# Performance work log

Hardware: AMD Instinct MI355X
Metric: run time of the kernel (lower is better)

The kernel has to match this reference:

```python
import jax, jax.numpy as jnp
import numpy as np

BN_EPS = 1e-5

def setup_inputs() -> dict:
    key = jax.random.key(0)
    B, C, T, N = 64, 1, 1024, 512
    weighted_fmri = jax.random.normal(key, (B, C, T, N), dtype=jnp.float32)
    bn_weight = jnp.ones((1,), dtype=jnp.float32)   # BatchNorm2d(1) affine weight
    bn_bias = jnp.zeros((1,), dtype=jnp.float32)    # BatchNorm2d(1) affine bias
    return {"weighted_fmri": weighted_fmri, "bn_weight": bn_weight, "bn_bias": bn_bias}


def reference(weighted_fmri, bn_weight, bn_bias):
    # weighted_fmri: [B, 1, T, N]. Original applies BatchNorm2d(1) per-sample
    # (batch of size 1 in training mode => normalize each sample by its own
    # mean/biased-var over (T, N)), then corrcoef over ROIs (columns).
    x = weighted_fmri
    mean = jnp.mean(x, axis=(1, 2, 3), keepdims=True)           # [B,1,1,1]
    var = jnp.mean((x - mean) ** 2, axis=(1, 2, 3), keepdims=True)  # biased var
    w = bn_weight.reshape(1, -1, 1, 1)
    b = bn_bias.reshape(1, -1, 1, 1)
    y = (x - mean) * jax.lax.rsqrt(var + BN_EPS) * w + b        # [B,1,T,N]

    X = y[:, 0]                                                 # [B,T,N]
    T = X.shape[1]
    # corrcoef(X.T): variables = N ROIs, observations = T timepoints
    Xc = X - jnp.mean(X, axis=1, keepdims=True)                 # center over time
    cov = jnp.einsum("btn,btm->bnm", Xc, Xc) / (T - 1)          # [B,N,N]
    d = jnp.sqrt(jnp.diagonal(cov, axis1=1, axis2=2))           # [B,N]
    corr = cov / (d[:, :, None] * d[:, None, :])
    return jnp.clip(corr, -1.0, 1.0)                            # [B,N,N]
```

## Files before the change

kernel.cpp:

```cpp
#include <hip/hip_runtime.h>
#include <hip/hip_bf16.h>

typedef __attribute__((ext_vector_type(8))) short bf16x8;
typedef __attribute__((ext_vector_type(4))) short s16x4;
typedef __attribute__((ext_vector_type(4))) float f32x4;

#define B_ 64
#define T_ 1024
#define N_ 512

#define FENCE() asm volatile("" ::: "memory")
#define VMWAIT(N) asm volatile("s_waitcnt vmcnt(" #N ")" ::: "memory")
#define BAR() __builtin_amdgcn_s_barrier()

__device__ __forceinline__ void async16(const void* g, void* l) {
  __builtin_amdgcn_global_load_lds(
      (const __attribute__((address_space(1))) unsigned int*)g,
      (__attribute__((address_space(3))) unsigned int*)l, 16, 0, 0);
}

__device__ __forceinline__ short f2bf(float f) {
  return __builtin_bit_cast(short, __float2bfloat16(f));
}
__device__ __forceinline__ float bf2f(short s) {
  return __builtin_bit_cast(float, ((unsigned)(unsigned short)s) << 16);
}

__global__ __launch_bounds__(256, 4) void k_prep(
    const float* __restrict__ X, short* __restrict__ XbT,
    float* __restrict__ amu, float* __restrict__ invd)
{
  __shared__ __align__(16) short tile[64][68];
  const int b   = blockIdx.y;
  const int n0  = blockIdx.x * 64;
  const int tid = threadIdx.x;
  const int nch = tid & 15;
  const int rg  = tid >> 4;

  float s[4] = {0.f,0.f,0.f,0.f}, q[4] = {0.f,0.f,0.f,0.f};

  for (int tt = 0; tt < 16; ++tt) {
    const int t0 = tt * 64;
    #pragma unroll
    for (int i = 0; i < 4; ++i) {
      const int tr = rg + i * 16;
      const float4 v = *(const float4*)&X[((size_t)b*T_ + t0 + tr)*N_ + n0 + nch*4];
      short bb[4];
      bb[0] = f2bf(v.x); bb[1] = f2bf(v.y); bb[2] = f2bf(v.z); bb[3] = f2bf(v.w);
      #pragma unroll
      for (int c = 0; c < 4; ++c) { float f = bf2f(bb[c]); s[c] += f; q[c] += f*f; }
      s16x4 pk = { bb[0], bb[1], bb[2], bb[3] };
      *(s16x4*)&tile[tr][nch*4] = pk;
    }
    __syncthreads();
    #pragma unroll
    for (int i = 0; i < 4; ++i) {
      const int n = rg + i * 16;
      s16x4 o = { tile[nch*4+0][n], tile[nch*4+1][n],
                  tile[nch*4+2][n], tile[nch*4+3][n] };
      *(s16x4*)&XbT[((size_t)b*N_ + n0 + n)*T_ + t0 + nch*4] = o;
    }
    __syncthreads();
  }

  float* fb = (float*)&tile[0][0];
  #pragma unroll
  for (int c = 0; c < 4; ++c) { fb[tid*8 + c] = s[c]; fb[tid*8 + 4 + c] = q[c]; }
  __syncthreads();
  if (tid < 64) {
    const int qc = tid >> 2, c = tid & 3;
    float cs = 0.f, sq = 0.f;
    #pragma unroll
    for (int g = 0; g < 16; ++g) {
      cs += fb[(g*16 + qc)*8 + c];
      sq += fb[(g*16 + qc)*8 + 4 + c];
    }
    const int n = n0 + qc*4 + c;
    amu[b*N_ + n]  = cs * (1.f/32.f);
    invd[b*N_ + n] = rsqrtf(fmaxf(sq - cs*cs*(1.f/1024.f), 1e-20f));
  }
}

__device__ __forceinline__ void compute_step(
    const short* A, const short* Bm, int aoff, int boff, int swz,
    f32x4 (&acc)[4][4])
{
  bf16x8 af[4], bfv[4];
  #pragma unroll
  for (int mi = 0; mi < 4; ++mi) af[mi] = *(const bf16x8*)&A[aoff + mi*512 + swz];
  #pragma unroll
  for (int ni = 0; ni < 4; ++ni) bfv[ni] = *(const bf16x8*)&Bm[boff + ni*512 + swz];
  #pragma unroll
  for (int mi = 0; mi < 4; ++mi)
    #pragma unroll
    for (int ni = 0; ni < 4; ++ni)
      acc[mi][ni] = __builtin_amdgcn_mfma_f32_16x16x32_bf16(
          af[mi], bfv[ni], acc[mi][ni], 0, 0, 0);
}

template<bool DIAG>
__device__ __forceinline__ void gram_main(
    const short* __restrict__ Xb,
    size_t ga0, size_t ga1, size_t gb0, size_t gb1,
    short (*ldsA)[4096], short (*ldsB)[4096],
    int tid, int aoff, int boff, int swz, f32x4 (&acc)[4][4])
{
  auto stg = [&](int bi, int kb) {
    char* la = (char*)ldsA[bi];
    async16(Xb + ga0 + kb, la + tid*16);
    async16(Xb + ga1 + kb, la + (tid+256)*16);
    if (!DIAG) {
      char* lb = (char*)ldsB[bi];
      async16(Xb + gb0 + kb, lb + tid*16);
      async16(Xb + gb1 + kb, lb + (tid+256)*16);
    }
  };
  auto cmp = [&](int bi) {
    compute_step(ldsA[bi], DIAG ? ldsA[bi] : ldsB[bi], aoff, boff, swz, acc);
  };

  stg(0, 0); stg(1, 32);
  #pragma unroll 1
  for (int it = 0; it < 10; ++it) {
    stg(2, (3*it + 2) * 32);
    if (DIAG) { VMWAIT(4); } else { VMWAIT(8); }
    BAR(); FENCE();
    cmp(0);
    FENCE(); BAR();
    stg(0, (3*it + 3) * 32);
    if (DIAG) { VMWAIT(4); } else { VMWAIT(8); }
    BAR(); FENCE();
    cmp(1);
    FENCE(); BAR();
    stg(1, (3*it + 4) * 32);
    if (DIAG) { VMWAIT(4); } else { VMWAIT(8); }
    BAR(); FENCE();
    cmp(2);
    FENCE(); BAR();
  }
  if (DIAG) { VMWAIT(2); } else { VMWAIT(4); }
  BAR(); FENCE();
  cmp(0);
  FENCE(); BAR();
  VMWAIT(0);
  BAR(); FENCE();
  cmp(1);
}

__global__ __launch_bounds__(256, 3) void k_gram(
    const short* __restrict__ XbT, const float* __restrict__ amu,
    const float* __restrict__ invd, float* __restrict__ out)
{
  __shared__ __align__(16) short ldsA[3][4096];
  __shared__ __align__(16) short ldsB[3][4096];

  const int bid = (blockIdx.x & 7) * 80 + (blockIdx.x >> 3);
  const int b = bid / 10;
  const int t = bid - b * 10;
  const int ip = (t >= 4) + (t >= 7) + (t >= 9);
  const int jp = ip + t - ((ip * (9 - ip)) >> 1);
  const int rowBase = ip * 128, colBase = jp * 128;
  const bool diag = (ip == jp);

  const int tid = threadIdx.x, lane = tid & 63, wave = tid >> 6;
  const int wr = wave >> 1, wc = wave & 1;
  const short* Xb = XbT + (size_t)b * N_ * T_;

  const int r0 = tid >> 2, cl = tid & 3;
  const int cg = cl ^ ((r0 >> 1) & 3);
  const size_t ga0 = (size_t)(rowBase + r0)      * T_ + cg * 8;
  const size_t ga1 = (size_t)(rowBase + r0 + 64) * T_ + cg * 8;
  const size_t gb0 = (size_t)(colBase + r0)      * T_ + cg * 8;
  const size_t gb1 = (size_t)(colBase + r0 + 64) * T_ + cg * 8;

  const int fr = lane & 15, kc = lane >> 4;
  const int swz  = (kc ^ ((fr >> 1) & 3)) * 8;
  const int aoff = (wr * 64 + fr) * 32;
  const int boff = (wc * 64 + fr) * 32;

  f32x4 acc[4][4] = {};
  if (diag) gram_main<true >(Xb, ga0, ga1, gb0, gb1, ldsA, ldsB, tid, aoff, boff, swz, acc);
  else      gram_main<false>(Xb, ga0, ga1, gb0, gb1, ldsA, ldsB, tid, aoff, boff, swz, acc);

  const int jc = colBase + wc * 64 + fr;
  float aj[4], dj[4];
  #pragma unroll
  for (int ni = 0; ni < 4; ++ni) {
    aj[ni] = amu [b*N_ + jc + ni*16];
    dj[ni] = invd[b*N_ + jc + ni*16];
  }
  #pragma unroll
  for (int mi = 0; mi < 4; ++mi) {
    const int ibase = rowBase + wr*64 + mi*16 + kc*4;
    float ai[4], di[4];
    #pragma unroll
    for (int r = 0; r < 4; ++r) {
      ai[r] = amu [b*N_ + ibase + r];
      di[r] = invd[b*N_ + ibase + r];
    }
    #pragma unroll
    for (int ni = 0; ni < 4; ++ni) {
      f32x4 g;
      #pragma unroll
      for (int r = 0; r < 4; ++r) {
        float v = (acc[mi][ni][r] - ai[r]*aj[ni]) * (di[r]*dj[ni]);
        g[r] = fminf(fmaxf(v, -1.f), 1.f);
      }
      const int J = jc + ni * 16;
      #pragma unroll
      for (int r = 0; r < 4; ++r)
        out[((size_t)b*N_ + ibase + r)*N_ + J] = g[r];
      if (!diag)
        *(f32x4*)&out[((size_t)b*N_ + J)*N_ + ibase] = g;
    }
  }
}

extern "C" void kernel_launch(void* const* d_in, const int* in_sizes, int n_in,
                              void* d_out, int out_size, void* d_ws, size_t ws_size,
                              hipStream_t stream) {
  const float* X = (const float*)d_in[0];
  float* out = (float*)d_out;

  char* ws = (char*)d_ws;
  short* XbT  = (short*)ws;
  size_t off  = (size_t)B_ * N_ * T_ * sizeof(short);
  float* amu  = (float*)(ws + off);
  float* invd = amu + B_ * N_;

  k_prep<<<dim3(N_/64, B_), 256, 0, stream>>>(X, XbT, amu, invd);
  k_gram<<<dim3(64 * 10), 256, 0, stream>>>(XbT, amu, invd, out);
}
```

Before: 68.24 us.

## Split gram tiles into 64x128 halves to double block count

```diff
diff --git a/kernel.cpp b/kernel.cpp
--- a/kernel.cpp
+++ b/kernel.cpp
@@ -81,64 +81,55 @@
   }
 }
 
-__device__ __forceinline__ void compute_step(
-    const short* A, const short* Bm, int aoff, int boff, int swz,
-    f32x4 (&acc)[4][4])
-{
-  bf16x8 af[4], bfv[4];
-  #pragma unroll
-  for (int mi = 0; mi < 4; ++mi) af[mi] = *(const bf16x8*)&A[aoff + mi*512 + swz];
-  #pragma unroll
-  for (int ni = 0; ni < 4; ++ni) bfv[ni] = *(const bf16x8*)&Bm[boff + ni*512 + swz];
-  #pragma unroll
-  for (int mi = 0; mi < 4; ++mi)
-    #pragma unroll
-    for (int ni = 0; ni < 4; ++ni)
-      acc[mi][ni] = __builtin_amdgcn_mfma_f32_16x16x32_bf16(
-          af[mi], bfv[ni], acc[mi][ni], 0, 0, 0);
-}
-
-template<bool DIAG>
+template<int L>
 __device__ __forceinline__ void gram_main(
     const short* __restrict__ Xb,
-    size_t ga0, size_t ga1, size_t gb0, size_t gb1,
-    short (*ldsA)[4096], short (*ldsB)[4096],
-    int tid, int aoff, int boff, int swz, f32x4 (&acc)[4][4])
+    size_t ga, size_t gb0, size_t gb1,
+    short (*lds)[6144], int tid, int aoff0, int boff0, f32x4 (&acc)[2][4])
 {
   auto stg = [&](int bi, int kb) {
-    char* la = (char*)ldsA[bi];
-    async16(Xb + ga0 + kb, la + tid*16);
-    async16(Xb + ga1 + kb, la + (tid+256)*16);
-    if (!DIAG) {
-      char* lb = (char*)ldsB[bi];
-      async16(Xb + gb0 + kb, lb + tid*16);
-      async16(Xb + gb1 + kb, lb + (tid+256)*16);
-    }
+    char* base = (char*)lds[bi];
+    async16(Xb + gb0 + kb, base + tid * 16);
+    async16(Xb + gb1 + kb, base + (tid + 256) * 16);
+    if (L == 3) async16(Xb + ga + kb, base + 8192 + tid * 16);
   };
   auto cmp = [&](int bi) {
-    compute_step(ldsA[bi], DIAG ? ldsA[bi] : ldsB[bi], aoff, boff, swz, acc);
+    const short* P = lds[bi];
+    bf16x8 af[2], bfv[4];
+    #pragma unroll
+    for (int mi = 0; mi < 2; ++mi) af[mi] = *(const bf16x8*)&P[aoff0 + mi * 512];
+    #pragma unroll
+    for (int ni = 0; ni < 4; ++ni) bfv[ni] = *(const bf16x8*)&P[boff0 + ni * 512];
+    __builtin_amdgcn_s_setprio(1);
+    #pragma unroll
+    for (int mi = 0; mi < 2; ++mi)
+      #pragma unroll
+      for (int ni = 0; ni < 4; ++ni)
+        acc[mi][ni] = __builtin_amdgcn_mfma_f32_16x16x32_bf16(
+            af[mi], bfv[ni], acc[mi][ni], 0, 0, 0);
+    __builtin_amdgcn_s_setprio(0);
   };
 
   stg(0, 0); stg(1, 32);
   #pragma unroll 1
   for (int it = 0; it < 10; ++it) {
     stg(2, (3*it + 2) * 32);
-    if (DIAG) { VMWAIT(4); } else { VMWAIT(8); }
+    if constexpr (L == 3) { VMWAIT(6); } else { VMWAIT(4); }
     BAR(); FENCE();
     cmp(0);
     FENCE(); BAR();
     stg(0, (3*it + 3) * 32);
-    if (DIAG) { VMWAIT(4); } else { VMWAIT(8); }
+    if constexpr (L == 3) { VMWAIT(6); } else { VMWAIT(4); }
     BAR(); FENCE();
     cmp(1);
     FENCE(); BAR();
     stg(1, (3*it + 4) * 32);
-    if (DIAG) { VMWAIT(4); } else { VMWAIT(8); }
+    if constexpr (L == 3) { VMWAIT(6); } else { VMWAIT(4); }
     BAR(); FENCE();
     cmp(2);
     FENCE(); BAR();
   }
-  if (DIAG) { VMWAIT(2); } else { VMWAIT(4); }
+  if constexpr (L == 3) { VMWAIT(3); } else { VMWAIT(2); }
   BAR(); FENCE();
   cmp(0);
   FENCE(); BAR();
@@ -147,40 +138,40 @@
   cmp(1);
 }
 
-__global__ __launch_bounds__(256, 3) void k_gram(
+__global__ __launch_bounds__(256, 4) void k_gram(
     const short* __restrict__ XbT, const float* __restrict__ amu,
     const float* __restrict__ invd, float* __restrict__ out)
 {
-  __shared__ __align__(16) short ldsA[3][4096];
-  __shared__ __align__(16) short ldsB[3][4096];
-
-  const int bid = (blockIdx.x & 7) * 80 + (blockIdx.x >> 3);
-  const int b = bid / 10;
-  const int t = bid - b * 10;
+  __shared__ __align__(16) short lds[3][6144];
+
+  const int bid = (blockIdx.x & 7) * 160 + (blockIdx.x >> 3);
+  const int b = bid / 20;
+  const int rem = bid - b * 20;
+  const int t = rem >> 1, h = rem & 1;
   const int ip = (t >= 4) + (t >= 7) + (t >= 9);
   const int jp = ip + t - ((ip * (9 - ip)) >> 1);
-  const int rowBase = ip * 128, colBase = jp * 128;
+  const int rowBase = ip * 128 + h * 64;
+  const int colBase = jp * 128;
   const bool diag = (ip == jp);
 
   const int tid = threadIdx.x, lane = tid & 63, wave = tid >> 6;
   const int wr = wave >> 1, wc = wave & 1;
+  const int fr = lane & 15, kc = lane >> 4;
+  const int swz = (kc ^ ((fr >> 1) & 3)) * 8;
   const short* Xb = XbT + (size_t)b * N_ * T_;
 
   const int r0 = tid >> 2, cl = tid & 3;
   const int cg = cl ^ ((r0 >> 1) & 3);
-  const size_t ga0 = (size_t)(rowBase + r0)      * T_ + cg * 8;
-  const size_t ga1 = (size_t)(rowBase + r0 + 64) * T_ + cg * 8;
   const size_t gb0 = (size_t)(colBase + r0)      * T_ + cg * 8;
   const size_t gb1 = (size_t)(colBase + r0 + 64) * T_ + cg * 8;
-
-  const int fr = lane & 15, kc = lane >> 4;
-  const int swz  = (kc ^ ((fr >> 1) & 3)) * 8;
-  const int aoff = (wr * 64 + fr) * 32;
-  const int boff = (wc * 64 + fr) * 32;
-
-  f32x4 acc[4][4] = {};
-  if (diag) gram_main<true >(Xb, ga0, ga1, gb0, gb1, ldsA, ldsB, tid, aoff, boff, swz, acc);
-  else      gram_main<false>(Xb, ga0, ga1, gb0, gb1, ldsA, ldsB, tid, aoff, boff, swz, acc);
+  const size_t ga  = (size_t)(rowBase + r0)      * T_ + cg * 8;
+
+  const int aoff0 = (diag ? h * 2048 : 4096) + (wr * 32 + fr) * 32 + swz;
+  const int boff0 = (wc * 64 + fr) * 32 + swz;
+
+  f32x4 acc[2][4] = {};
+  if (diag) gram_main<2>(Xb, ga, gb0, gb1, lds, tid, aoff0, boff0, acc);
+  else      gram_main<3>(Xb, ga, gb0, gb1, lds, tid, aoff0, boff0, acc);
 
   const int jc = colBase + wc * 64 + fr;
   float aj[4], dj[4];
@@ -190,8 +181,8 @@
     dj[ni] = invd[b*N_ + jc + ni*16];
   }
   #pragma unroll
-  for (int mi = 0; mi < 4; ++mi) {
-    const int ibase = rowBase + wr*64 + mi*16 + kc*4;
+  for (int mi = 0; mi < 2; ++mi) {
+    const int ibase = rowBase + wr*32 + mi*16 + kc*4;
     float ai[4], di[4];
     #pragma unroll
     for (int r = 0; r < 4; ++r) {
@@ -229,5 +220,5 @@
   float* invd = amu + B_ * N_;
 
   k_prep<<<dim3(N_/64, B_), 256, 0, stream>>>(X, XbT, amu, invd);
-  k_gram<<<dim3(64 * 10), 256, 0, stream>>>(XbT, amu, invd, out);
-}
+  k_gram<<<dim3(1280), 256, 0, stream>>>(XbT, amu, invd, out);
+}
```

After: 75.25 us. 1.1x slower.

## Software-pipeline LDS fragment reads with MFMA using double register buffers

Applied to the files above, without the earlier changes.

```diff
diff --git a/kernel.cpp b/kernel.cpp
--- a/kernel.cpp
+++ b/kernel.cpp
@@ -11,6 +11,7 @@
 
 #define FENCE() asm volatile("" ::: "memory")
 #define VMWAIT(N) asm volatile("s_waitcnt vmcnt(" #N ")" ::: "memory")
+#define LGKM0()  asm volatile("s_waitcnt lgkmcnt(0)" ::: "memory")
 #define BAR() __builtin_amdgcn_s_barrier()
 
 __device__ __forceinline__ void async16(const void* g, void* l) {
@@ -81,78 +82,87 @@
   }
 }
 
-__device__ __forceinline__ void compute_step(
-    const short* A, const short* Bm, int aoff, int boff, int swz,
-    f32x4 (&acc)[4][4])
-{
-  bf16x8 af[4], bfv[4];
-  #pragma unroll
-  for (int mi = 0; mi < 4; ++mi) af[mi] = *(const bf16x8*)&A[aoff + mi*512 + swz];
-  #pragma unroll
-  for (int ni = 0; ni < 4; ++ni) bfv[ni] = *(const bf16x8*)&Bm[boff + ni*512 + swz];
-  #pragma unroll
-  for (int mi = 0; mi < 4; ++mi)
-    #pragma unroll
-    for (int ni = 0; ni < 4; ++ni)
-      acc[mi][ni] = __builtin_amdgcn_mfma_f32_16x16x32_bf16(
-          af[mi], bfv[ni], acc[mi][ni], 0, 0, 0);
-}
-
-template<bool DIAG>
+template<int L>
 __device__ __forceinline__ void gram_main(
     const short* __restrict__ Xb,
     size_t ga0, size_t ga1, size_t gb0, size_t gb1,
-    short (*ldsA)[4096], short (*ldsB)[4096],
-    int tid, int aoff, int boff, int swz, f32x4 (&acc)[4][4])
+    short* lds, int tid, int aoff, int boff, f32x4 (&acc)[4][4])
 {
-  auto stg = [&](int bi, int kb) {
-    char* la = (char*)ldsA[bi];
-    async16(Xb + ga0 + kb, la + tid*16);
-    async16(Xb + ga1 + kb, la + (tid+256)*16);
-    if (!DIAG) {
-      char* lb = (char*)ldsB[bi];
-      async16(Xb + gb0 + kb, lb + tid*16);
-      async16(Xb + gb1 + kb, lb + (tid+256)*16);
+  auto stg = [&](int c3, int kb) {
+    char* base = (char*)lds + c3 * 16384;
+    async16(Xb + gb0 + kb, base + tid * 16);
+    async16(Xb + gb1 + kb, base + (tid + 256) * 16);
+    if constexpr (L == 4) {
+      async16(Xb + ga0 + kb, base + 8192 + tid * 16);
+      async16(Xb + ga1 + kb, base + 8192 + (tid + 256) * 16);
     }
   };
-  auto cmp = [&](int bi) {
-    compute_step(ldsA[bi], DIAG ? ldsA[bi] : ldsB[bi], aoff, boff, swz, acc);
+  auto rd = [&](int c3, bf16x8 (&A)[4], bf16x8 (&B)[4]) {
+    const short* P = lds + c3 * 8192;
+    #pragma unroll
+    for (int i = 0; i < 4; ++i) A[i] = *(const bf16x8*)&P[aoff + i * 512];
+    #pragma unroll
+    for (int i = 0; i < 4; ++i) B[i] = *(const bf16x8*)&P[boff + i * 512];
   };
-
-  stg(0, 0); stg(1, 32);
+  auto mm = [&](bf16x8 (&A)[4], bf16x8 (&B)[4]) {
+    __builtin_amdgcn_s_setprio(1);
+    #pragma unroll
+    for (int mi = 0; mi < 4; ++mi)
+      #pragma unroll
+      for (int ni = 0; ni < 4; ++ni)
+        acc[mi][ni] = __builtin_amdgcn_mfma_f32_16x16x32_bf16(
+            A[mi], B[ni], acc[mi][ni], 0, 0, 0);
+    __builtin_amdgcn_s_setprio(0);
+  };
+  #define WAITL() do { if constexpr (L == 4) VMWAIT(4); else VMWAIT(2); } while (0)
+
+  bf16x8 A0[4], B0[4], A1[4], B1[4];
+
+  stg(0, 0); stg(1, 32); stg(2, 64);
+  if constexpr (L == 4) VMWAIT(8); else VMWAIT(4);
+  BAR(); FENCE();
+  rd(0, A0, B0);
+  LGKM0();
+
+  int c3 = 0;
   #pragma unroll 1
-  for (int it = 0; it < 10; ++it) {
-    stg(2, (3*it + 2) * 32);
-    if (DIAG) { VMWAIT(4); } else { VMWAIT(8); }
-    BAR(); FENCE();
-    cmp(0);
-    FENCE(); BAR();
-    stg(0, (3*it + 3) * 32);
-    if (DIAG) { VMWAIT(4); } else { VMWAIT(8); }
-    BAR(); FENCE();
-    cmp(1);
-    FENCE(); BAR();
-    stg(1, (3*it + 4) * 32);
-    if (DIAG) { VMWAIT(4); } else { VMWAIT(8); }
-    BAR(); FENCE();
-    cmp(2);
-    FENCE(); BAR();
-  }
-  if (DIAG) { VMWAIT(2); } else { VMWAIT(4); }
-  BAR(); FENCE();
-  cmp(0);
-  FENCE(); BAR();
-  VMWAIT(0);
-  BAR(); FENCE();
-  cmp(1);
+  for (int t = 0; t < 28; t += 2) {
+    const int c3a = (c3 == 2) ? 0 : c3 + 1;
+    const int c3b = (c3a == 2) ? 0 : c3a + 1;
+    WAITL(); BAR(); FENCE();
+    stg(c3, (t + 3) * 32);
+    rd(c3a, A1, B1);
+    mm(A0, B0);
+    LGKM0();
+    WAITL(); BAR(); FENCE();
+    stg(c3a, (t + 4) * 32);
+    rd(c3b, A0, B0);
+    mm(A1, B1);
+    LGKM0();
+    c3 = c3b;
+  }
+  WAITL(); BAR(); FENCE();
+  stg(1, 31 * 32);
+  rd(2, A1, B1);
+  mm(A0, B0);
+  LGKM0();
+  WAITL(); BAR(); FENCE();
+  rd(0, A0, B0);
+  mm(A1, B1);
+  LGKM0();
+  VMWAIT(0); BAR(); FENCE();
+  rd(1, A1, B1);
+  mm(A0, B0);
+  LGKM0();
+  mm(A1, B1);
+  #undef WAITL
 }
 
 __global__ __launch_bounds__(256, 3) void k_gram(
     const short* __restrict__ XbT, const float* __restrict__ amu,
     const float* __restrict__ invd, float* __restrict__ out)
 {
-  __shared__ __align__(16) short ldsA[3][4096];
-  __shared__ __align__(16) short ldsB[3][4096];
+  __shared__ __align__(16) short lds[3][8192];
 
   const int bid = (blockIdx.x & 7) * 80 + (blockIdx.x >> 3);
   const int b = bid / 10;
@@ -168,19 +178,19 @@
 
   const int r0 = tid >> 2, cl = tid & 3;
   const int cg = cl ^ ((r0 >> 1) & 3);
+  const size_t gb0 = (size_t)(colBase + r0)      * T_ + cg * 8;
+  const size_t gb1 = (size_t)(colBase + r0 + 64) * T_ + cg * 8;
   const size_t ga0 = (size_t)(rowBase + r0)      * T_ + cg * 8;
   const size_t ga1 = (size_t)(rowBase + r0 + 64) * T_ + cg * 8;
-  const size_t gb0 = (size_t)(colBase + r0)      * T_ + cg * 8;
-  const size_t gb1 = (size_t)(colBase + r0 + 64) * T_ + cg * 8;
 
   const int fr = lane & 15, kc = lane >> 4;
   const int swz  = (kc ^ ((fr >> 1) & 3)) * 8;
-  const int aoff = (wr * 64 + fr) * 32;
-  const int boff = (wc * 64 + fr) * 32;
+  const int boff = (wc * 64 + fr) * 32 + swz;
+  const int aoff = (diag ? 0 : 4096) + (wr * 64 + fr) * 32 + swz;
 
   f32x4 acc[4][4] = {};
-  if (diag) gram_main<true >(Xb, ga0, ga1, gb0, gb1, ldsA, ldsB, tid, aoff, boff, swz, acc);
-  else      gram_main<false>(Xb, ga0, ga1, gb0, gb1, ldsA, ldsB, tid, aoff, boff, swz, acc);
+  if (diag) gram_main<2>(Xb, ga0, ga1, gb0, gb1, &lds[0][0], tid, aoff, boff, acc);
+  else      gram_main<4>(Xb, ga0, ga1, gb0, gb1, &lds[0][0], tid, aoff, boff, acc);
 
   const int jc = colBase + wc * 64 + fr;
   float aj[4], dj[4];
```

Result: slower. 72.23 us (+5.9%).

## Narrow prep tiles to 32 columns and software-pipeline global loads

Applied to the files above, without the earlier changes.

```diff
diff --git a/kernel.cpp b/kernel.cpp
--- a/kernel.cpp
+++ b/kernel.cpp
@@ -11,6 +11,7 @@
 
 #define FENCE() asm volatile("" ::: "memory")
 #define VMWAIT(N) asm volatile("s_waitcnt vmcnt(" #N ")" ::: "memory")
+#define LGKM0()  asm volatile("s_waitcnt lgkmcnt(0)" ::: "memory")
 #define BAR() __builtin_amdgcn_s_barrier()
 
 __device__ __forceinline__ void async16(const void* g, void* l) {
@@ -30,55 +31,86 @@
     const float* __restrict__ X, short* __restrict__ XbT,
     float* __restrict__ amu, float* __restrict__ invd)
 {
-  __shared__ __align__(16) short tile[64][68];
+  __shared__ __align__(16) char smraw[8192];
+  short (*tile)[36] = (short(*)[36])smraw;
+
   const int b   = blockIdx.y;
-  const int n0  = blockIdx.x * 64;
+  const int n0  = blockIdx.x * 32;
   const int tid = threadIdx.x;
-  const int nch = tid & 15;
-  const int rg  = tid >> 4;
+  const int nch = tid & 7,  rg = tid >> 3;
+  const int sch = tid & 15, sn = tid >> 4;
 
   float s[4] = {0.f,0.f,0.f,0.f}, q[4] = {0.f,0.f,0.f,0.f};
-
-  for (int tt = 0; tt < 16; ++tt) {
-    const int t0 = tt * 64;
-    #pragma unroll
-    for (int i = 0; i < 4; ++i) {
-      const int tr = rg + i * 16;
-      const float4 v = *(const float4*)&X[((size_t)b*T_ + t0 + tr)*N_ + n0 + nch*4];
-      short bb[4];
-      bb[0] = f2bf(v.x); bb[1] = f2bf(v.y); bb[2] = f2bf(v.z); bb[3] = f2bf(v.w);
-      #pragma unroll
-      for (int c = 0; c < 4; ++c) { float f = bf2f(bb[c]); s[c] += f; q[c] += f*f; }
-      s16x4 pk = { bb[0], bb[1], bb[2], bb[3] };
-      *(s16x4*)&tile[tr][nch*4] = pk;
-    }
-    __syncthreads();
-    #pragma unroll
-    for (int i = 0; i < 4; ++i) {
-      const int n = rg + i * 16;
-      s16x4 o = { tile[nch*4+0][n], tile[nch*4+1][n],
-                  tile[nch*4+2][n], tile[nch*4+3][n] };
-      *(s16x4*)&XbT[((size_t)b*N_ + n0 + n)*T_ + t0 + nch*4] = o;
-    }
-    __syncthreads();
-  }
-
-  float* fb = (float*)&tile[0][0];
+  const float* base0 = X + (size_t)b * T_ * N_ + n0 + nch * 4;
+
+  float4 vA0, vA1, vB0, vB1;
+
+  #define LOADI(u0, u1, tt) do {                                        \
+    const float* p_ = base0 + (size_t)((tt) * 64 + rg) * N_;            \
+    u0 = *(const float4*)p_;                                            \
+    u1 = *(const float4*)(p_ + (size_t)32 * N_);                        \
+  } while (0)
+
+  #define WRITEI(u0, u1) do {                                           \
+    const float4* uu_[2] = { &u0, &u1 };                                \
+    _Pragma("unroll")                                                   \
+    for (int i = 0; i < 2; ++i) {                                       \
+      const float4 u = *uu_[i];                                         \
+      short b0 = f2bf(u.x), b1 = f2bf(u.y), b2 = f2bf(u.z), b3 = f2bf(u.w); \
+      float f0 = bf2f(b0), f1 = bf2f(b1), f2 = bf2f(b2), f3 = bf2f(b3); \
+      s[0] += f0; q[0] += f0*f0;  s[1] += f1; q[1] += f1*f1;            \
+      s[2] += f2; q[2] += f2*f2;  s[3] += f3; q[3] += f3*f3;            \
+      s16x4 pk = { b0, b1, b2, b3 };                                    \
+      *(s16x4*)&tile[rg + i * 32][nch * 4] = pk;                        \
+    }                                                                   \
+  } while (0)
+
+  #define STOREI(tt) do {                                               \
+    _Pragma("unroll")                                                   \
+    for (int i = 0; i < 2; ++i) {                                       \
+      const int n_ = sn + i * 16;                                       \
+      s16x4 o = { tile[sch*4+0][n_], tile[sch*4+1][n_],                 \
+                  tile[sch*4+2][n_], tile[sch*4+3][n_] };               \
+      *(s16x4*)&XbT[((size_t)b*N_ + n0 + n_)*T_ + (tt)*64 + sch*4] = o; \
+    }                                                                   \
+  } while (0)
+
+  LOADI(vA0, vA1, 0);
+  #pragma unroll 1
+  for (int tt = 0; tt < 16; tt += 2) {
+    WRITEI(vA0, vA1);
+    if (tt + 1 < 16) LOADI(vB0, vB1, tt + 1);
+    LGKM0(); BAR(); FENCE();
+    STOREI(tt);
+    LGKM0(); BAR(); FENCE();
+
+    WRITEI(vB0, vB1);
+    if (tt + 2 < 16) LOADI(vA0, vA1, tt + 2);
+    LGKM0(); BAR(); FENCE();
+    STOREI(tt + 1);
+    LGKM0(); BAR(); FENCE();
+  }
+
+  __syncthreads();
+  float* fb = (float*)smraw;
   #pragma unroll
   for (int c = 0; c < 4; ++c) { fb[tid*8 + c] = s[c]; fb[tid*8 + 4 + c] = q[c]; }
   __syncthreads();
-  if (tid < 64) {
-    const int qc = tid >> 2, c = tid & 3;
+  if (tid < 32) {
+    const int nc = tid >> 2, c = tid & 3;
     float cs = 0.f, sq = 0.f;
-    #pragma unroll
-    for (int g = 0; g < 16; ++g) {
-      cs += fb[(g*16 + qc)*8 + c];
-      sq += fb[(g*16 + qc)*8 + 4 + c];
-    }
-    const int n = n0 + qc*4 + c;
+    #pragma unroll 1
+    for (int r = 0; r < 32; ++r) {
+      cs += fb[(r*8 + nc)*8 + c];
+      sq += fb[(r*8 + nc)*8 + 4 + c];
+    }
+    const int n = n0 + nc*4 + c;
     amu[b*N_ + n]  = cs * (1.f/32.f);
     invd[b*N_ + n] = rsqrtf(fmaxf(sq - cs*cs*(1.f/1024.f), 1e-20f));
   }
+  #undef LOADI
+  #undef WRITEI
+  #undef STOREI
 }
 
 __device__ __forceinline__ void compute_step(
@@ -106,13 +138,13 @@
     int tid, int aoff, int boff, int swz, f32x4 (&acc)[4][4])
 {
   auto stg = [&](int bi, int kb) {
-    char* la = (char*)ldsA[bi];
-    async16(Xb + ga0 + kb, la + tid*16);
-    async16(Xb + ga1 + kb, la + (tid+256)*16);
+    char* la_ = (char*)ldsA[bi];
+    async16(Xb + ga0 + kb, la_ + tid*16);
+    async16(Xb + ga1 + kb, la_ + (tid+256)*16);
     if (!DIAG) {
-      char* lb = (char*)ldsB[bi];
-      async16(Xb + gb0 + kb, lb + tid*16);
-      async16(Xb + gb1 + kb, lb + (tid+256)*16);
+      char* lb_ = (char*)ldsB[bi];
+      async16(Xb + gb0 + kb, lb_ + tid*16);
+      async16(Xb + gb1 + kb, lb_ + (tid+256)*16);
     }
   };
   auto cmp = [&](int bi) {
@@ -123,22 +155,22 @@
   #pragma unroll 1
   for (int it = 0; it < 10; ++it) {
     stg(2, (3*it + 2) * 32);
-    if (DIAG) { VMWAIT(4); } else { VMWAIT(8); }
+    if constexpr (DIAG) { VMWAIT(4); } else { VMWAIT(8); }
     BAR(); FENCE();
     cmp(0);
     FENCE(); BAR();
     stg(0, (3*it + 3) * 32);
-    if (DIAG) { VMWAIT(4); } else { VMWAIT(8); }
+    if constexpr (DIAG) { VMWAIT(4); } else { VMWAIT(8); }
     BAR(); FENCE();
     cmp(1);
     FENCE(); BAR();
     stg(1, (3*it + 4) * 32);
-    if (DIAG) { VMWAIT(4); } else { VMWAIT(8); }
+    if constexpr (DIAG) { VMWAIT(4); } else { VMWAIT(8); }
     BAR(); FENCE();
     cmp(2);
     FENCE(); BAR();
   }
-  if (DIAG) { VMWAIT(2); } else { VMWAIT(4); }
+  if constexpr (DIAG) { VMWAIT(2); } else { VMWAIT(4); }
   BAR(); FENCE();
   cmp(0);
   FENCE(); BAR();
@@ -168,10 +200,10 @@
 
   const int r0 = tid >> 2, cl = tid & 3;
   const int cg = cl ^ ((r0 >> 1) & 3);
+  const size_t gb0 = (size_t)(colBase + r0)      * T_ + cg * 8;
+  const size_t gb1 = (size_t)(colBase + r0 + 64) * T_ + cg * 8;
   const size_t ga0 = (size_t)(rowBase + r0)      * T_ + cg * 8;
   const size_t ga1 = (size_t)(rowBase + r0 + 64) * T_ + cg * 8;
-  const size_t gb0 = (size_t)(colBase + r0)      * T_ + cg * 8;
-  const size_t gb1 = (size_t)(colBase + r0 + 64) * T_ + cg * 8;
 
   const int fr = lane & 15, kc = lane >> 4;
   const int swz  = (kc ^ ((fr >> 1) & 3)) * 8;
@@ -228,6 +260,6 @@
   float* amu  = (float*)(ws + off);
   float* invd = amu + B_ * N_;
 
-  k_prep<<<dim3(N_/64, B_), 256, 0, stream>>>(X, XbT, amu, invd);
+  k_prep<<<dim3(16, 64), 256, 0, stream>>>(X, XbT, amu, invd);
   k_gram<<<dim3(64 * 10), 256, 0, stream>>>(XbT, amu, invd, out);
 }
```

Result: slower. 71.20 us (+4.3%).
